# Performance work log

Hardware: AMD Instinct MI355X
Metric: run time of the kernel (lower is better)

The kernel has to match this reference:

```python
import jax, jax.numpy as jnp
import numpy as np

DATA_BITS = 57
SHIFT_BITS = 6
BATCH = 1_000_000


def setup_inputs() -> dict:
    key = jax.random.key(0)
    kx, ks = jax.random.split(key)
    # binary spike bits in {0,1}, stored as float32 (SNN convention)
    X = jax.random.randint(kx, (BATCH, DATA_BITS), 0, 2).astype(jnp.float32)
    shift = jax.random.randint(ks, (BATCH, SHIFT_BITS), 0, 2).astype(jnp.float32)
    return {"X": X, "shift": shift}


def _barrel_shift_right_sticky(X, shift):
    # X: [..., 57] bits, shift: [..., 6] bits (MSB first)
    zeros = jnp.zeros_like(X[..., 0:1])
    current = X
    sticky_accum = zeros
    for layer in range(SHIFT_BITS):
        shift_amt = 2 ** (SHIFT_BITS - 1 - layer)  # 32,16,8,4,2,1 (all <= 57)
        s_bit = shift[..., layer:layer + 1]  # [..., 1]
        # VecORTree over the bits that would be shifted out
        layer_sticky = jnp.max(current[..., DATA_BITS - shift_amt:], axis=-1, keepdims=True)
        # VecMUX(s, layer_sticky, 0) = s * layer_sticky
        layer_sticky_selected = s_bit * layer_sticky
        # VecOR accumulate (binary OR == max for {0,1})
        sticky_accum = jnp.maximum(sticky_accum, layer_sticky_selected)
        # right shift by shift_amt: prepend zeros, drop low bits (shift_amt < 57 always)
        pad = jnp.zeros(current.shape[:-1] + (shift_amt,), dtype=current.dtype)
        shifted = jnp.concatenate([pad, current[..., :-shift_amt]], axis=-1)
        # VecMUX(s, shifted, current)
        current = s_bit * shifted + (1.0 - s_bit) * current
    return current, sticky_accum


def reference(X, shift):
    return _barrel_shift_right_sticky(X, shift)
```

## Files before the change

### kernel.cpp

```cpp
#include <hip/hip_runtime.h>
#include <stdint.h>

#define DATA_BITS 57
#define SHIFT_BITS 6
#define ROWS_PER_BLOCK 256
#define BLOCK 256
#define TILE_FLOATS (ROWS_PER_BLOCK * DATA_BITS)
#define TILE_VEC (TILE_FLOATS / 4)
#define NSTAGE (TILE_VEC / 64)
#define MASK57 ((1ULL << DATA_BITS) - 1ULL)

typedef float floatx4 __attribute__((ext_vector_type(4)));

__device__ __forceinline__ void gload_lds16(const float4* g, float4* l) {
    __builtin_amdgcn_global_load_lds(
        (const __attribute__((address_space(1))) void*)g,
        (__attribute__((address_space(3))) void*)l,
        16, 0, 0);
}

__device__ __forceinline__ floatx4 expand(const unsigned long long* masks, int p) {
    int row = p / DATA_BITS;
    int col = p - row * DATA_BITS;
    unsigned long long m = masks[row] >> col;
    if (col > DATA_BITS - 4)
        m |= masks[row + 1] << (DATA_BITS - col);
    uint32_t c = (uint32_t)m;
    floatx4 f;
    f.x = __uint_as_float((0u - (c        & 1u)) & 0x3F800000u);
    f.y = __uint_as_float((0u - ((c >> 1) & 1u)) & 0x3F800000u);
    f.z = __uint_as_float((0u - ((c >> 2) & 1u)) & 0x3F800000u);
    f.w = __uint_as_float((0u - ((c >> 3) & 1u)) & 0x3F800000u);
    return f;
}

__global__ __launch_bounds__(BLOCK, 2) void barrel57_kernel(
    const float* __restrict__ X, const float* __restrict__ S,
    float* __restrict__ outCur, float* __restrict__ outSticky,
    int batch)
{
    __shared__ float tile[TILE_FLOATS];
    __shared__ unsigned long long maskOut[ROWS_PER_BLOCK + 2];

    const int t    = threadIdx.x;
    const int wave = t >> 6;
    const int lane = t & 63;
    const long long blockRow0 = (long long)blockIdx.x * ROWS_PER_BLOCK;
    const long long xBase = blockRow0 * DATA_BITS;
    const long long row   = blockRow0 + t;
    const bool fullBlock  = (blockRow0 + ROWS_PER_BLOCK <= (long long)batch);

    float sv[SHIFT_BITS];
    if (row < (long long)batch) {
        const float* sp = S + row * SHIFT_BITS;
        #pragma unroll
        for (int l = 0; l < SHIFT_BITS; ++l) sv[l] = sp[l];
    } else {
        #pragma unroll
        for (int l = 0; l < SHIFT_BITS; ++l) sv[l] = 0.0f;
    }

    float4* tileV = (float4*)tile;
    if (fullBlock) {
        const float4* Xv = (const float4*)X + (xBase >> 2);
        #pragma unroll
        for (int j = 0; j < (NSTAGE + 3) / 4; ++j) {
            int i = wave + 4 * j;
            if (i < NSTAGE) gload_lds16(Xv + i * 64 + lane, tileV + i * 64);
        }
    } else {
        const long long totalV = (long long)batch * DATA_BITS / 4;
        const long long vBase  = xBase >> 2;
        #pragma unroll
        for (int j = 0; j < (NSTAGE + 3) / 4; ++j) {
            int i = wave + 4 * j;
            if (i < NSTAGE) {
                long long gi = vBase + i * 64 + lane;
                if (gi >= totalV) gi = totalV - 1;
                gload_lds16((const float4*)X + gi, tileV + i * 64);
            }
        }
    }
    if (t < 2) maskOut[ROWS_PER_BLOCK + t] = 0ULL;
    __syncthreads();

    {
        unsigned long long outm = 0ULL;
        if (row < (long long)batch) {
            const float* r = &tile[t * DATA_BITS];
            uint32_t lo = 0u, hi = 0u;
            #pragma unroll
            for (int k = 0; k < 32; ++k)
                lo |= ((__float_as_uint(r[k]) >> 23) & 1u) << k;
            #pragma unroll
            for (int k = 32; k < DATA_BITS; ++k)
                hi |= ((__float_as_uint(r[k]) >> 23) & 1u) << (k - 32);
            unsigned long long mask = ((unsigned long long)hi << 32) | lo;

            int s = 0;
            #pragma unroll
            for (int l = 0; l < SHIFT_BITS; ++l)
                s |= (int)(sv[l] != 0.0f) << (SHIFT_BITS - 1 - l);

            outm = (mask << s) & MASK57;
            unsigned long long dropped = (s >= DATA_BITS) ? mask : (mask >> (DATA_BITS - s));
            __builtin_nontemporal_store((dropped != 0ULL) ? 1.0f : 0.0f, &outSticky[row]);
        }
        maskOut[t] = outm;
    }
    __syncthreads();

    floatx4* Ov = (floatx4*)outCur + (xBase >> 2);
    if (fullBlock) {
        #pragma unroll
        for (int k = 0; k < TILE_VEC / BLOCK; ++k) {
            int i = t + k * BLOCK;
            __builtin_nontemporal_store(expand(maskOut, i * 4), &Ov[i]);
        }
        if (t < TILE_VEC - (TILE_VEC / BLOCK) * BLOCK) {
            int i = t + (TILE_VEC / BLOCK) * BLOCK;
            __builtin_nontemporal_store(expand(maskOut, i * 4), &Ov[i]);
        }
    } else {
        const long long totalV = (long long)batch * DATA_BITS / 4;
        const long long vBase  = xBase >> 2;
        for (int i = t; i < TILE_VEC; i += BLOCK)
            if (vBase + i < totalV)
                __builtin_nontemporal_store(expand(maskOut, i * 4), &Ov[i]);
    }
}

extern "C" void kernel_launch(void* const* d_in, const int* in_sizes, int n_in,
                              void* d_out, int out_size, void* d_ws, size_t ws_size,
                              hipStream_t stream) {
    const float* X = (const float*)d_in[0];
    const float* S = (const float*)d_in[1];
    const int batch = in_sizes[1] / SHIFT_BITS;
    float* outCur = (float*)d_out;
    float* outSticky = outCur + (long long)batch * DATA_BITS;

    const int grid = (batch + ROWS_PER_BLOCK - 1) / ROWS_PER_BLOCK;
    barrel57_kernel<<<grid, BLOCK, 0, stream>>>(X, S, outCur, outSticky, batch);
}
```

Measured before the change: 72.94 us.

## Pack input bits per wave with ballot instead of staging floats in LDS

Each wave now processes 64 rows on its own. It loads X with coalesced scalar loads into registers and turns each 64-float slab into a 64-bit word with __ballot. Lanes then pull their 57-bit row mask out of a small per-wave LDS word array. The goal is to drop the 58KB LDS tile and the block-wide __syncthreads, which allows higher occupancy (launch bounds 8) and cheaper bit extraction. It relies on wave-local LDS visibility through s_waitcnt fences only, and it gives up the async global_load_lds path.

```diff
diff --git a/kernel.cpp b/kernel.cpp
--- a/kernel.cpp
+++ b/kernel.cpp
@@ -3,20 +3,19 @@
 
 #define DATA_BITS 57
 #define SHIFT_BITS 6
-#define ROWS_PER_BLOCK 256
 #define BLOCK 256
-#define TILE_FLOATS (ROWS_PER_BLOCK * DATA_BITS)
-#define TILE_VEC (TILE_FLOATS / 4)
-#define NSTAGE (TILE_VEC / 64)
+#define WAVES_PER_BLOCK 4
+#define ROWS_PER_WAVE 64
+#define WAVE_FLOATS (ROWS_PER_WAVE * DATA_BITS)
+#define NLOAD (WAVE_FLOATS / 64)
+#define CHUNK 19
+#define WAVE_VEC (WAVE_FLOATS / 4)
 #define MASK57 ((1ULL << DATA_BITS) - 1ULL)
 
 typedef float floatx4 __attribute__((ext_vector_type(4)));
 
-__device__ __forceinline__ void gload_lds16(const float4* g, float4* l) {
-    __builtin_amdgcn_global_load_lds(
-        (const __attribute__((address_space(1))) void*)g,
-        (__attribute__((address_space(3))) void*)l,
-        16, 0, 0);
+__device__ __forceinline__ void lds_fence() {
+    asm volatile("s_waitcnt lgkmcnt(0)" ::: "memory");
 }
 
 __device__ __forceinline__ floatx4 expand(const unsigned long long* masks, int p) {
@@ -34,99 +33,112 @@
     return f;
 }
 
-__global__ __launch_bounds__(BLOCK, 2) void barrel57_kernel(
+__global__ __launch_bounds__(BLOCK, 8) void barrel57_kernel(
     const float* __restrict__ X, const float* __restrict__ S,
     float* __restrict__ outCur, float* __restrict__ outSticky,
     int batch)
 {
-    __shared__ float tile[TILE_FLOATS];
-    __shared__ unsigned long long maskOut[ROWS_PER_BLOCK + 2];
+    __shared__ unsigned long long words[WAVES_PER_BLOCK][NLOAD + 2];
+    __shared__ unsigned long long maskOut[WAVES_PER_BLOCK][ROWS_PER_WAVE + 2];
 
     const int t    = threadIdx.x;
-    const int wave = t >> 6;
+    const int wv   = t >> 6;
     const int lane = t & 63;
-    const long long blockRow0 = (long long)blockIdx.x * ROWS_PER_BLOCK;
-    const long long xBase = blockRow0 * DATA_BITS;
-    const long long row   = blockRow0 + t;
-    const bool fullBlock  = (blockRow0 + ROWS_PER_BLOCK <= (long long)batch);
+    const long long W = (long long)blockIdx.x * WAVES_PER_BLOCK + wv;
+    const long long nWavesFull = (long long)batch / ROWS_PER_WAVE;
+    const long long row = W * ROWS_PER_WAVE + lane;
 
-    float sv[SHIFT_BITS];
-    if (row < (long long)batch) {
-        const float* sp = S + row * SHIFT_BITS;
-        #pragma unroll
-        for (int l = 0; l < SHIFT_BITS; ++l) sv[l] = sp[l];
-    } else {
-        #pragma unroll
-        for (int l = 0; l < SHIFT_BITS; ++l) sv[l] = 0.0f;
+    if (W >= nWavesFull) {
+        if (W * ROWS_PER_WAVE >= (long long)batch) return;
+        const long long totalF = (long long)batch * DATA_BITS;
+        const long long eBase  = W * WAVE_FLOATS;
+        if (lane < 2) { words[wv][NLOAD + lane] = 0ULL; maskOut[wv][ROWS_PER_WAVE + lane] = 0ULL; }
+        for (int k = 0; k < NLOAD; ++k) {
+            long long e = eBase + k * 64 + lane;
+            float x = (e < totalF) ? X[e] : 0.0f;
+            unsigned long long bal = __ballot(x != 0.0f);
+            if (lane == 0) words[wv][k] = bal;
+        }
+        lds_fence();
+        unsigned long long outm = 0ULL;
+        if (row < (long long)batch) {
+            int bit0 = lane * DATA_BITS, w0 = bit0 >> 6, off = bit0 & 63;
+            unsigned long long mask = words[wv][w0] >> off;
+            if (off) mask |= words[wv][w0 + 1] << (64 - off);
+            mask &= MASK57;
+            int s = 0;
+            for (int l = 0; l < SHIFT_BITS; ++l)
+                s |= (int)(S[row * SHIFT_BITS + l] != 0.0f) << (SHIFT_BITS - 1 - l);
+            outm = (mask << s) & MASK57;
+            unsigned long long dropped = (s >= DATA_BITS) ? mask : (mask >> (DATA_BITS - s));
+            outSticky[row] = (dropped != 0ULL) ? 1.0f : 0.0f;
+        }
+        maskOut[wv][lane] = outm;
+        lds_fence();
+        for (int k = 0; k <= NLOAD / 4; ++k) {
+            int i = k * 64 + lane;
+            if (i < WAVE_VEC) {
+                long long e = eBase + i * 4;
+                if (e + 3 < totalF) {
+                    *((floatx4*)outCur + (eBase >> 2) + i) = expand(maskOut[wv], i * 4);
+                } else {
+                    floatx4 f = expand(maskOut[wv], i * 4);
+                    for (int j = 0; j < 4; ++j) if (e + j < totalF) outCur[e + j] = f[j];
+                }
+            }
+        }
+        return;
     }
 
-    float4* tileV = (float4*)tile;
-    if (fullBlock) {
-        const float4* Xv = (const float4*)X + (xBase >> 2);
+    const float* sp = S + row * SHIFT_BITS;
+    float sv[SHIFT_BITS];
+    #pragma unroll
+    for (int l = 0; l < SHIFT_BITS; ++l) sv[l] = sp[l];
+
+    if (lane < 2) { words[wv][NLOAD + lane] = 0ULL; maskOut[wv][ROWS_PER_WAVE + lane] = 0ULL; }
+
+    const float* Xp = X + W * WAVE_FLOATS;
+    #pragma unroll
+    for (int c = 0; c < 3; ++c) {
+        float f[CHUNK];
         #pragma unroll
-        for (int j = 0; j < (NSTAGE + 3) / 4; ++j) {
-            int i = wave + 4 * j;
-            if (i < NSTAGE) gload_lds16(Xv + i * 64 + lane, tileV + i * 64);
-        }
-    } else {
-        const long long totalV = (long long)batch * DATA_BITS / 4;
-        const long long vBase  = xBase >> 2;
+        for (int j = 0; j < CHUNK; ++j) f[j] = Xp[(c * CHUNK + j) * 64 + lane];
         #pragma unroll
-        for (int j = 0; j < (NSTAGE + 3) / 4; ++j) {
-            int i = wave + 4 * j;
-            if (i < NSTAGE) {
-                long long gi = vBase + i * 64 + lane;
-                if (gi >= totalV) gi = totalV - 1;
-                gload_lds16((const float4*)X + gi, tileV + i * 64);
-            }
+        for (int j = 0; j < CHUNK; ++j) {
+            unsigned long long bal = __ballot(f[j] != 0.0f);
+            if (lane == 0) words[wv][c * CHUNK + j] = bal;
         }
     }
-    if (t < 2) maskOut[ROWS_PER_BLOCK + t] = 0ULL;
-    __syncthreads();
+    lds_fence();
 
     {
-        unsigned long long outm = 0ULL;
-        if (row < (long long)batch) {
-            const float* r = &tile[t * DATA_BITS];
-            uint32_t lo = 0u, hi = 0u;
-            #pragma unroll
-            for (int k = 0; k < 32; ++k)
-                lo |= ((__float_as_uint(r[k]) >> 23) & 1u) << k;
-            #pragma unroll
-            for (int k = 32; k < DATA_BITS; ++k)
-                hi |= ((__float_as_uint(r[k]) >> 23) & 1u) << (k - 32);
-            unsigned long long mask = ((unsigned long long)hi << 32) | lo;
+        const int bit0 = lane * DATA_BITS;
+        const int w0 = bit0 >> 6, off = bit0 & 63;
+        unsigned long long mask = words[wv][w0] >> off;
+        if (off) mask |= words[wv][w0 + 1] << (64 - off);
+        mask &= MASK57;
 
-            int s = 0;
-            #pragma unroll
-            for (int l = 0; l < SHIFT_BITS; ++l)
-                s |= (int)(sv[l] != 0.0f) << (SHIFT_BITS - 1 - l);
+        int s = 0;
+        #pragma unroll
+        for (int l = 0; l < SHIFT_BITS; ++l)
+            s |= (int)(sv[l] != 0.0f) << (SHIFT_BITS - 1 - l);
 
-            outm = (mask << s) & MASK57;
-            unsigned long long dropped = (s >= DATA_BITS) ? mask : (mask >> (DATA_BITS - s));
-            __builtin_nontemporal_store((dropped != 0ULL) ? 1.0f : 0.0f, &outSticky[row]);
-        }
-        maskOut[t] = outm;
+        unsigned long long outm = (mask << s) & MASK57;
+        unsigned long long dropped = (s >= DATA_BITS) ? mask : (mask >> (DATA_BITS - s));
+        __builtin_nontemporal_store((dropped != 0ULL) ? 1.0f : 0.0f, &outSticky[row]);
+        maskOut[wv][lane] = outm;
     }
-    __syncthreads();
+    lds_fence();
 
-    floatx4* Ov = (floatx4*)outCur + (xBase >> 2);
-    if (fullBlock) {
-        #pragma unroll
-        for (int k = 0; k < TILE_VEC / BLOCK; ++k) {
-            int i = t + k * BLOCK;
-            __builtin_nontemporal_store(expand(maskOut, i * 4), &Ov[i]);
-        }
-        if (t < TILE_VEC - (TILE_VEC / BLOCK) * BLOCK) {
-            int i = t + (TILE_VEC / BLOCK) * BLOCK;
-            __builtin_nontemporal_store(expand(maskOut, i * 4), &Ov[i]);
-        }
-    } else {
-        const long long totalV = (long long)batch * DATA_BITS / 4;
-        const long long vBase  = xBase >> 2;
-        for (int i = t; i < TILE_VEC; i += BLOCK)
-            if (vBase + i < totalV)
-                __builtin_nontemporal_store(expand(maskOut, i * 4), &Ov[i]);
+    floatx4* Ov = (floatx4*)outCur + ((W * WAVE_FLOATS) >> 2);
+    #pragma unroll
+    for (int k = 0; k < WAVE_VEC / 64; ++k) {
+        int i = k * 64 + lane;
+        __builtin_nontemporal_store(expand(maskOut[wv], i * 4), &Ov[i]);
+    }
+    if (lane < WAVE_VEC - (WAVE_VEC / 64) * 64) {
+        int i = (WAVE_VEC / 64) * 64 + lane;
+        __builtin_nontemporal_store(expand(maskOut[wv], i * 4), &Ov[i]);
     }
 }
 
@@ -139,6 +151,7 @@
     float* outCur = (float*)d_out;
     float* outSticky = outCur + (long long)batch * DATA_BITS;
 
-    const int grid = (batch + ROWS_PER_BLOCK - 1) / ROWS_PER_BLOCK;
+    const long long nWaves = ((long long)batch + ROWS_PER_WAVE - 1) / ROWS_PER_WAVE;
+    const int grid = (int)((nWaves + WAVES_PER_BLOCK - 1) / WAVES_PER_BLOCK);
     barrel57_kernel<<<grid, BLOCK, 0, stream>>>(X, S, outCur, outSticky, batch);
 }
```

Result: faster. 71.28 us (-2.3%).
